# Kernel tuning notes

Measured on AMD Instinct MI355X. Metric: run time of the kernel, lower is better.

Reference implementation:

```python
import jax, jax.numpy as jnp
import numpy as np

T, I, H = 4096, 2048, 2048


def setup_inputs() -> dict:
    key = jax.random.key(0)
    ks = jax.random.split(key, 7)
    s = 0.075
    return {
        "x": jax.random.normal(ks[0], (1, T, I), dtype=jnp.float32),
        "W_ih": jax.random.normal(ks[1], (4 * H, I), dtype=jnp.float32) * s,
        "W_hh": jax.random.normal(ks[2], (4 * H, H), dtype=jnp.float32) * s,
        "b_ih": jax.random.normal(ks[3], (4 * H,), dtype=jnp.float32) * s,
        "b_hh": jax.random.normal(ks[4], (4 * H,), dtype=jnp.float32) * s,
        "Wo": jax.random.normal(ks[5], (I, H), dtype=jnp.float32) * s,
        "bo": jax.random.normal(ks[6], (I,), dtype=jnp.float32) * s,
    }


def reference(x, W_ih, W_hh, b_ih, b_hh, Wo, bo):
    xs = x[0]  # [T, I]  (batch dim of 1 squeezed, as in original)
    # Precompute input projections for all timesteps in one big GEMM: [T, 4H]
    gx = xs @ W_ih.T + (b_ih + b_hh)

    def step(carry, gxt):
        h, c = carry  # [H], [H]
        g = gxt + W_hh @ h  # [4H]; PyTorch gate order: i, f, g, o
        i_g, f_g, g_g, o_g = jnp.split(g, 4)
        c_new = jax.nn.sigmoid(f_g) * c + jax.nn.sigmoid(i_g) * jnp.tanh(g_g)
        h_new = jax.nn.sigmoid(o_g) * jnp.tanh(c_new)
        return (h_new, c_new), h_new

    h0 = jnp.zeros((H,), dtype=x.dtype)
    c0 = jnp.zeros((H,), dtype=x.dtype)
    _, hs = jax.lax.scan(step, (h0, c0), gx)  # hs: [T, H]

    out = jax.nn.sigmoid(hs @ Wo.T + bo)  # [T, I]
    return out[None]  # [1, T, I]
```

## Files before the change

### kernel.cpp

```cpp
#include <hip/hip_runtime.h>

#define T_STEPS 4096
#define IDIM 2048
#define HDIM 2048
#define G4DIM 8192

typedef __attribute__((ext_vector_type(8))) short short8;
typedef __attribute__((ext_vector_type(4))) float f32x4;
typedef __attribute__((ext_vector_type(2))) float f32x2;

__device__ __forceinline__ unsigned short f2bf(float f) {
  unsigned int u = __float_as_uint(f);
  u += 0x7fffu + ((u >> 16) & 1u);
  return (unsigned short)(u >> 16);
}
__device__ __forceinline__ float bf2f(unsigned short h) {
  return __uint_as_float(((unsigned int)h) << 16);
}

template <int ACT_SIGMOID, int OUT_BF16>
__global__ __launch_bounds__(256) void gemm_bt(
    const float* __restrict__ A, const float* __restrict__ B,
    const float* __restrict__ bias, void* __restrict__ Cout,
    int M, int N, int K)
{
  __shared__ short Ah[64][40];
  __shared__ short Al[64][40];
  __shared__ short Bh[64][40];
  __shared__ short Bl[64][40];
  const int tid  = threadIdx.x;
  const int wave = tid >> 6, lane = tid & 63;
  const int bn = blockIdx.x * 64, bm = blockIdx.y * 64;
  const int srow = tid >> 2, sc8 = (tid & 3) * 8;
  const int wm = (wave >> 1) * 32, wn = (wave & 1) * 32;
  const int lq = lane >> 4, lr = lane & 15;
  f32x4 acc[2][2] = {};

  for (int k0 = 0; k0 < K; k0 += 32) {
    __syncthreads();
    {
      const float* src = A + (size_t)(bm + srow) * K + k0 + sc8;
      float4 v0 = *(const float4*)(src);
      float4 v1 = *(const float4*)(src + 4);
      float vv[8] = {v0.x, v0.y, v0.z, v0.w, v1.x, v1.y, v1.z, v1.w};
      short8 vh, vl;
      #pragma unroll
      for (int i = 0; i < 8; ++i) {
        unsigned short hb = f2bf(vv[i]);
        vh[i] = (short)hb;
        vl[i] = (short)f2bf(vv[i] - bf2f(hb));
      }
      *(short8*)&Ah[srow][sc8] = vh;
      *(short8*)&Al[srow][sc8] = vl;
    }
    {
      const float* src = B + (size_t)(bn + srow) * K + k0 + sc8;
      float4 v0 = *(const float4*)(src);
      float4 v1 = *(const float4*)(src + 4);
      float vv[8] = {v0.x, v0.y, v0.z, v0.w, v1.x, v1.y, v1.z, v1.w};
      short8 vh, vl;
      #pragma unroll
      for (int i = 0; i < 8; ++i) {
        unsigned short hb = f2bf(vv[i]);
        vh[i] = (short)hb;
        vl[i] = (short)f2bf(vv[i] - bf2f(hb));
      }
      *(short8*)&Bh[srow][sc8] = vh;
      *(short8*)&Bl[srow][sc8] = vl;
    }
    __syncthreads();

    short8 ah0 = *(const short8*)&Ah[wm +      lr][lq * 8];
    short8 al0 = *(const short8*)&Al[wm +      lr][lq * 8];
    short8 ah1 = *(const short8*)&Ah[wm + 16 + lr][lq * 8];
    short8 al1 = *(const short8*)&Al[wm + 16 + lr][lq * 8];
    short8 bh0 = *(const short8*)&Bh[wn +      lr][lq * 8];
    short8 bl0 = *(const short8*)&Bl[wn +      lr][lq * 8];
    short8 bh1 = *(const short8*)&Bh[wn + 16 + lr][lq * 8];
    short8 bl1 = *(const short8*)&Bl[wn + 16 + lr][lq * 8];

    acc[0][0] = __builtin_amdgcn_mfma_f32_16x16x32_bf16(ah0, bh0, acc[0][0], 0, 0, 0);
    acc[0][0] = __builtin_amdgcn_mfma_f32_16x16x32_bf16(ah0, bl0, acc[0][0], 0, 0, 0);
    acc[0][0] = __builtin_amdgcn_mfma_f32_16x16x32_bf16(al0, bh0, acc[0][0], 0, 0, 0);

    acc[0][1] = __builtin_amdgcn_mfma_f32_16x16x32_bf16(ah0, bh1, acc[0][1], 0, 0, 0);
    acc[0][1] = __builtin_amdgcn_mfma_f32_16x16x32_bf16(ah0, bl1, acc[0][1], 0, 0, 0);
    acc[0][1] = __builtin_amdgcn_mfma_f32_16x16x32_bf16(al0, bh1, acc[0][1], 0, 0, 0);

    acc[1][0] = __builtin_amdgcn_mfma_f32_16x16x32_bf16(ah1, bh0, acc[1][0], 0, 0, 0);
    acc[1][0] = __builtin_amdgcn_mfma_f32_16x16x32_bf16(ah1, bl0, acc[1][0], 0, 0, 0);
    acc[1][0] = __builtin_amdgcn_mfma_f32_16x16x32_bf16(al1, bh0, acc[1][0], 0, 0, 0);

    acc[1][1] = __builtin_amdgcn_mfma_f32_16x16x32_bf16(ah1, bh1, acc[1][1], 0, 0, 0);
    acc[1][1] = __builtin_amdgcn_mfma_f32_16x16x32_bf16(ah1, bl1, acc[1][1], 0, 0, 0);
    acc[1][1] = __builtin_amdgcn_mfma_f32_16x16x32_bf16(al1, bh1, acc[1][1], 0, 0, 0);
  }

  #pragma unroll
  for (int mi = 0; mi < 2; ++mi) {
    #pragma unroll
    for (int ni = 0; ni < 2; ++ni) {
      #pragma unroll
      for (int rr = 0; rr < 4; ++rr) {
        int row = bm + wm + mi * 16 + lq * 4 + rr;
        int col = bn + wn + ni * 16 + lr;
        float v = acc[mi][ni][rr];
        if (bias) v += bias[col];
        if (ACT_SIGMOID) v = 1.f / (1.f + __expf(-v));
        if (OUT_BF16)
          ((unsigned short*)Cout)[(size_t)row * N + col] = f2bf(v);
        else
          ((float*)Cout)[(size_t)row * N + col] = v;
      }
    }
  }
}

__global__ __launch_bounds__(1024, 4) void lstm_scan(
    const float* __restrict__ Whh,
    const float* __restrict__ b_ih, const float* __restrict__ b_hh,
    const unsigned short* __restrict__ gx,
    float* __restrict__ hs)
{
  const int b   = blockIdx.x;
  const int tid = threadIdx.x;
  const int u   = tid & 7;
  const int kc  = tid >> 3;
  const int wv  = tid >> 6;

  f32x2 w2[4][8];
  #pragma unroll
  for (int g = 0; g < 4; ++g) {
    const float* wp = Whh + (size_t)(g * HDIM + b * 8 + u) * HDIM + kc * 16;
    #pragma unroll
    for (int i = 0; i < 4; ++i) {
      float4 v = *(const float4*)(wp + 4 * i);
      w2[g][2 * i]     = f32x2{v.x, v.y};
      w2[g][2 * i + 1] = f32x2{v.z, v.w};
    }
  }
  float bias_r = 0.f;
  if (tid < 32) {
    int br = (tid >> 3) * HDIM + b * 8 + (tid & 7);
    bias_r = b_ih[br] + b_hh[br];
  }
  float cval = 0.f;

  __shared__ float h_lds[128 * 20];
  __shared__ float partials[2][16][33];
  unsigned int* hs_u = (unsigned int*)hs;

  for (int t = 0; t < T_STEPS; ++t) {
    float gxv = 0.f;
    if (tid < 32)
      gxv = bf2f(gx[(size_t)t * G4DIM + (tid >> 3) * HDIM + b * 8 + (tid & 7)]);

    f32x2 h2w;
    if (t > 0) {
      const unsigned int* p = hs_u + (size_t)(t - 1) * HDIM + tid * 2;
      unsigned int u0, u1;
      for (;;) {
        u0 = __hip_atomic_load(p + 0, __ATOMIC_RELAXED, __HIP_MEMORY_SCOPE_AGENT);
        u1 = __hip_atomic_load(p + 1, __ATOMIC_RELAXED, __HIP_MEMORY_SCOPE_AGENT);
        if (u0 != 0xAAAAAAAAu && u1 != 0xAAAAAAAAu) break;
        __builtin_amdgcn_s_sleep(1);
      }
      h2w = f32x2{__uint_as_float(u0), __uint_as_float(u1)};
    } else {
      h2w = f32x2{0.f, 0.f};
    }

    *(f32x2*)&h_lds[kc * 20 + u * 2] = h2w;

    f32x2 acc0{0.f, 0.f}, acc1{0.f, 0.f}, acc2{0.f, 0.f}, acc3{0.f, 0.f};
    #pragma unroll
    for (int i = 0; i < 4; ++i) {
      float4 hv = *(const float4*)&h_lds[kc * 20 + i * 4];
      f32x2 ha{hv.x, hv.y}, hb{hv.z, hv.w};
      acc0 += w2[0][2 * i] * ha;  acc0 += w2[0][2 * i + 1] * hb;
      acc1 += w2[1][2 * i] * ha;  acc1 += w2[1][2 * i + 1] * hb;
      acc2 += w2[2][2 * i] * ha;  acc2 += w2[2][2 * i + 1] * hb;
      acc3 += w2[3][2 * i] * ha;  acc3 += w2[3][2 * i + 1] * hb;
    }
    float s0 = acc0[0] + acc0[1];
    float s1 = acc1[0] + acc1[1];
    float s2 = acc2[0] + acc2[1];
    float s3 = acc3[0] + acc3[1];
    #pragma unroll
    for (int m = 8; m <= 32; m <<= 1) {
      s0 += __shfl_xor(s0, m, 64);
      s1 += __shfl_xor(s1, m, 64);
      s2 += __shfl_xor(s2, m, 64);
      s3 += __shfl_xor(s3, m, 64);
    }
    if ((tid & 56) == 0) {
      partials[t & 1][wv][0 * 8 + u] = s0;
      partials[t & 1][wv][1 * 8 + u] = s1;
      partials[t & 1][wv][2 * 8 + u] = s2;
      partials[t & 1][wv][3 * 8 + u] = s3;
    }
    __syncthreads();

    if (tid < 64) {
      float gval = 0.f;
      if (tid < 32) {
        float s = gxv + bias_r;
        #pragma unroll
        for (int q = 0; q < 16; ++q) s += partials[t & 1][q][tid];
        gval = s;
      }
      float g_i = __shfl(gval, tid);
      float g_f = __shfl(gval, tid + 8);
      float g_g = __shfl(gval, tid + 16);
      float g_o = __shfl(gval, tid + 24);
      if (tid < 8) {
        float is = 1.f / (1.f + __expf(-g_i));
        float fs = 1.f / (1.f + __expf(-g_f));
        float os = 1.f / (1.f + __expf(-g_o));
        float e2 = __expf(-2.f * fabsf(g_g));
        float tg = (1.f - e2) / (1.f + e2);
        tg = (g_g < 0.f) ? -tg : tg;
        float cn = fs * cval + is * tg;
        cval = cn;
        float ec = __expf(-2.f * fabsf(cn));
        float tc = (1.f - ec) / (1.f + ec);
        tc = (cn < 0.f) ? -tc : tc;
        float hn = os * tc;
        __hip_atomic_store(hs_u + (size_t)t * HDIM + b * 8 + tid,
                           __float_as_uint(hn),
                           __ATOMIC_RELAXED, __HIP_MEMORY_SCOPE_AGENT);
      }
    }
  }
}

extern "C" void kernel_launch(void* const* d_in, const int* in_sizes, int n_in,
                              void* d_out, int out_size, void* d_ws, size_t ws_size,
                              hipStream_t stream) {
  (void)in_sizes; (void)n_in; (void)out_size; (void)ws_size;
  const float* x    = (const float*)d_in[0];
  const float* W_ih = (const float*)d_in[1];
  const float* W_hh = (const float*)d_in[2];
  const float* b_ih = (const float*)d_in[3];
  const float* b_hh = (const float*)d_in[4];
  const float* Wo   = (const float*)d_in[5];
  const float* bo   = (const float*)d_in[6];
  float* out = (float*)d_out;

  char* ws = (char*)d_ws;
  unsigned short* gx = (unsigned short*)ws;
  float* hs = (float*)(ws + (size_t)T_STEPS * G4DIM * 2);

  hipMemsetAsync(hs, 0xAA, (size_t)T_STEPS * HDIM * sizeof(float), stream);

  gemm_bt<0, 1><<<dim3(G4DIM / 64, T_STEPS / 64), 256, 0, stream>>>(
      x, W_ih, nullptr, gx, T_STEPS, G4DIM, IDIM);

  lstm_scan<<<256, 1024, 0, stream>>>(W_hh, b_ih, b_hh, gx, hs);

  gemm_bt<1, 0><<<dim3(IDIM / 64, T_STEPS / 64), 256, 0, stream>>>(
      hs, Wo, bo, out, T_STEPS, IDIM, HDIM);
}
```

Baseline: 12.63 ms.

## Replace per-step block barrier with per-wave LDS sequence flags in LSTM scan

```diff
diff --git a/kernel.cpp b/kernel.cpp
--- a/kernel.cpp
+++ b/kernel.cpp
@@ -127,6 +127,7 @@
   const int u   = tid & 7;
   const int kc  = tid >> 3;
   const int wv  = tid >> 6;
+  const int lane = tid & 63;
 
   f32x2 w2[4][8];
   #pragma unroll
@@ -147,25 +148,39 @@
   float cval = 0.f;
 
   __shared__ float h_lds[128 * 20];
-  __shared__ float partials[2][16][33];
+  __shared__ float partials[2][32][17];
+  __shared__ int   seqs[2][16];
+  if (tid < 32) ((int*)seqs)[tid] = -1;
+  __syncthreads();
+
   unsigned int* hs_u = (unsigned int*)hs;
 
+  const unsigned short* gxp = gx + (tid >> 3) * HDIM + b * 8 + (tid & 7);
+  unsigned short gxr_cur = 0, gxr_nxt = 0;
+  if (tid < 32) gxr_cur = gxp[0];
+
   for (int t = 0; t < T_STEPS; ++t) {
-    float gxv = 0.f;
-    if (tid < 32)
-      gxv = bf2f(gx[(size_t)t * G4DIM + (tid >> 3) * HDIM + b * 8 + (tid & 7)]);
+    const int buf = t & 1;
+    if (tid < 32 && t + 1 < T_STEPS)
+      gxr_nxt = gxp[(size_t)(t + 1) * G4DIM];
 
     f32x2 h2w;
     if (t > 0) {
-      const unsigned int* p = hs_u + (size_t)(t - 1) * HDIM + tid * 2;
-      unsigned int u0, u1;
+      const unsigned long long* p =
+          (const unsigned long long*)(hs_u + (size_t)(t - 1) * HDIM + tid * 2);
+      unsigned long long a =
+          __hip_atomic_load(p, __ATOMIC_RELAXED, __HIP_MEMORY_SCOPE_AGENT);
       for (;;) {
-        u0 = __hip_atomic_load(p + 0, __ATOMIC_RELAXED, __HIP_MEMORY_SCOPE_AGENT);
-        u1 = __hip_atomic_load(p + 1, __ATOMIC_RELAXED, __HIP_MEMORY_SCOPE_AGENT);
-        if (u0 != 0xAAAAAAAAu && u1 != 0xAAAAAAAAu) break;
+        unsigned long long nb =
+            __hip_atomic_load(p, __ATOMIC_RELAXED, __HIP_MEMORY_SCOPE_AGENT);
+        unsigned int lo = (unsigned int)a, hi = (unsigned int)(a >> 32);
+        if (lo != 0xAAAAAAAAu && hi != 0xAAAAAAAAu) {
+          h2w = f32x2{__uint_as_float(lo), __uint_as_float(hi)};
+          break;
+        }
         __builtin_amdgcn_s_sleep(1);
-      }
-      h2w = f32x2{__uint_as_float(u0), __uint_as_float(u1)};
+        a = nb;
+      }
     } else {
       h2w = f32x2{0.f, 0.f};
     }
@@ -194,19 +209,32 @@
       s3 += __shfl_xor(s3, m, 64);
     }
     if ((tid & 56) == 0) {
-      partials[t & 1][wv][0 * 8 + u] = s0;
-      partials[t & 1][wv][1 * 8 + u] = s1;
-      partials[t & 1][wv][2 * 8 + u] = s2;
-      partials[t & 1][wv][3 * 8 + u] = s3;
-    }
-    __syncthreads();
+      partials[buf][0 * 8 + u][wv] = s0;
+      partials[buf][1 * 8 + u][wv] = s1;
+      partials[buf][2 * 8 + u][wv] = s2;
+      partials[buf][3 * 8 + u][wv] = s3;
+    }
+    if (lane == 0)
+      __hip_atomic_store(&seqs[buf][wv], t, __ATOMIC_RELEASE,
+                         __HIP_MEMORY_SCOPE_WORKGROUP);
 
     if (tid < 64) {
+      const int sidx = lane & 15;
+      for (;;) {
+        int sv = __hip_atomic_load(&seqs[buf][sidx], __ATOMIC_ACQUIRE,
+                                   __HIP_MEMORY_SCOPE_WORKGROUP);
+        if (__all(sv >= t)) break;
+      }
+      __builtin_amdgcn_s_setprio(1);
       float gval = 0.f;
       if (tid < 32) {
-        float s = gxv + bias_r;
+        float s = bf2f(gxr_cur) + bias_r;
+        const float* pr = &partials[buf][tid][0];
         #pragma unroll
-        for (int q = 0; q < 16; ++q) s += partials[t & 1][q][tid];
+        for (int i = 0; i < 4; ++i) {
+          float4 v = *(const float4*)(pr + 4 * i);
+          s += (v.x + v.y) + (v.z + v.w);
+        }
         gval = s;
       }
       float g_i = __shfl(gval, tid);
@@ -230,7 +258,9 @@
                            __float_as_uint(hn),
                            __ATOMIC_RELAXED, __HIP_MEMORY_SCOPE_AGENT);
       }
-    }
+      __builtin_amdgcn_s_setprio(0);
+    }
+    gxr_cur = gxr_nxt;
   }
 }
 
```

After: 12.87 ms. No clear change (+1.9%).
